# Kernel optimization log

Measured on AMD Instinct MI355X. Metric: run time of the kernel, lower is better.

The kernel has to match this reference:

```python
import jax, jax.numpy as jnp
import numpy as np

ROPE_BASE = 100.0  # CroCo/InfiniteVGGT-style 2D RoPE base

def _rope_1d(sub, pos, base=ROPE_BASE):
    # sub: (B,H,N,half), pos: (B,N) float
    half = sub.shape[-1]
    quarter = half // 2
    inv_freq = 1.0 / (base ** (jnp.arange(quarter, dtype=jnp.float32) / quarter))
    ang = pos[:, None, :, None] * inv_freq  # (B,1,N,quarter)
    cos, sin = jnp.cos(ang), jnp.sin(ang)
    x1, x2 = sub[..., :quarter], sub[..., quarter:]
    return jnp.concatenate([x1 * cos - x2 * sin, x1 * sin + x2 * cos], axis=-1)

def rope_2d(t, positions):
    # t: (B,H,N,Dh); positions: (B,N,2) int (y,x)
    Dh = t.shape[-1]
    half = Dh // 2
    pos_f = positions.astype(t.dtype)
    y = _rope_1d(t[..., :half], pos_f[..., 0])
    x = _rope_1d(t[..., half:], pos_f[..., 1])
    return jnp.concatenate([y, x], axis=-1)

def setup_inputs() -> dict:
    key = jax.random.key(0)
    k1, k2, k3, k4 = jax.random.split(key, 4)
    B, N, C, H = 2, 2048, 1024, 16
    x = jax.random.normal(k1, (B, N, C), dtype=jnp.float32)
    positions = jax.random.randint(k2, (B, N, 2), 0, 64, dtype=jnp.int32)
    qkv_w = jax.random.normal(k3, (3 * C, C), dtype=jnp.float32) * (C ** -0.5)
    proj_w = jax.random.normal(k4, (C, C), dtype=jnp.float32) * (C ** -0.5)
    proj_b = jnp.zeros((C,), dtype=jnp.float32)
    return {"x": x, "positions": positions, "qkv_w": qkv_w, "proj_w": proj_w, "proj_b": proj_b}

def reference(x, positions, qkv_w, proj_w, proj_b):
    B, N, C = x.shape
    H = 16
    Dh = C // H
    scale = Dh ** -0.5
    qkv = (x @ qkv_w.T).reshape(B, N, 3, H, Dh).transpose(2, 0, 3, 1, 4)  # (3,B,H,N,Dh)
    q, k, v = qkv[0], qkv[1], qkv[2]
    q = rope_2d(q, positions)
    k = rope_2d(k, positions)
    attn = jnp.einsum('bhnd,bhmd->bhnm', q, k) * scale  # (B,H,N,N)
    attn = jax.nn.softmax(attn, axis=-1)
    out = jnp.einsum('bhnm,bhmd->bhnd', attn, v)  # (B,H,N,Dh)
    out = out.transpose(0, 2, 1, 3).reshape(B, N, C)
    return out @ proj_w.T + proj_b
```

## Files before the change

### kernel.cpp

```cpp
#include <hip/hip_runtime.h>
#include <cmath>

typedef unsigned short u16;
typedef unsigned int   u32;
typedef __attribute__((ext_vector_type(8))) __bf16 bf16x8;
typedef __attribute__((ext_vector_type(2))) __bf16 bf16x2;
typedef __attribute__((ext_vector_type(4))) float  f32x4;
typedef __attribute__((ext_vector_type(2))) unsigned int u32x2;

constexpr int BB = 2, SEQ = 2048, CH = 1024, NH = 16, DH = 64;

__device__ inline u16 f2bf(float f) {
    u32 u = __builtin_bit_cast(u32, f);
    u += 0x7FFF + ((u >> 16) & 1);
    return (u16)(u >> 16);
}
__device__ inline float bf2f(u16 b) { return __builtin_bit_cast(float, (u32)b << 16); }
__device__ inline u32 pkbf(float a, float b) {
#if __has_builtin(__builtin_amdgcn_cvt_pk_bf16_f32)
    bf16x2 r = __builtin_amdgcn_cvt_pk_bf16_f32(a, b);
    return __builtin_bit_cast(u32, r);
#else
    return (u32)f2bf(a) | ((u32)f2bf(b) << 16);
#endif
}
__device__ inline float fexp2(float x) {
#if __has_builtin(__builtin_amdgcn_exp2f)
    return __builtin_amdgcn_exp2f(x);
#else
    return exp2f(x);
#endif
}

__device__ inline void pl32swap(u32& a, u32& b) {
#if __has_builtin(__builtin_amdgcn_permlane32_swap)
    u32x2 r = __builtin_amdgcn_permlane32_swap(a, b, false, false);
    a = r.x; b = r.y;
#else
    const int ln = threadIdx.x & 63;
    u32 ax = (u32)__shfl_xor((int)a, 32), bx = (u32)__shfl_xor((int)b, 32);
    u32 na = (ln & 32) ? bx : a;
    u32 nb = (ln & 32) ? b : ax;
    a = na; b = nb;
#endif
}
__device__ inline void pl16swap(u32& a, u32& b) {
#if __has_builtin(__builtin_amdgcn_permlane16_swap)
    u32x2 r = __builtin_amdgcn_permlane16_swap(a, b, false, false);
    a = r.x; b = r.y;
#else
    const int ln = threadIdx.x & 63;
    u32 ax = (u32)__shfl_xor((int)a, 16), bx = (u32)__shfl_xor((int)b, 16);
    u32 na = (ln & 16) ? bx : a;
    u32 nb = (ln & 16) ? b : ax;
    a = na; b = nb;
#endif
}

__device__ inline void gld_lds16(const void* g, void* l) {
    __builtin_amdgcn_global_load_lds((const __attribute__((address_space(1))) void*)g,
                                     (__attribute__((address_space(3))) void*)l, 16, 0, 0);
}
__device__ inline f32x4 mfma16(bf16x8 a, bf16x8 b, f32x4 c) {
    return __builtin_amdgcn_mfma_f32_16x16x32_bf16(a, b, c, 0, 0, 0);
}
__device__ inline bf16x8 ld_frag(const u16* p) {
    return __builtin_bit_cast(bf16x8, *(const uint4*)p);
}

__global__ __launch_bounds__(256) void convert_kernel(const float* __restrict__ x,
                                                      const float* __restrict__ wq,
                                                      const float* __restrict__ wp,
                                                      u16* __restrict__ xb,
                                                      u16* __restrict__ wqb,
                                                      u16* __restrict__ wpb,
                                                      float2* __restrict__ tabq,
                                                      float2* __restrict__ tabk) {
    const int q = blockIdx.x * 256 + threadIdx.x;
    if (q >= 2097152) {
        const int idx = q - 2097152;
        if (idx < 1024) {
            const int p = idx >> 4, i = idx & 15;
            const float f = exp2f(-(float)i * 0.41524101186092f);
            float s, c;
            sincosf((float)p * f, &s, &c);
            tabk[idx] = make_float2(c, s);
            tabq[idx] = make_float2(c * 0.18033688011112042f,
                                    s * 0.18033688011112042f);
        }
        return;
    }
    const float* src; u16* dst; int idx;
    if (q < 1048576)            { src = x;  dst = xb;  idx = q; }
    else if (q < 1048576+786432){ src = wq; dst = wqb; idx = q - 1048576; }
    else                        { src = wp; dst = wpb; idx = q - 1048576 - 786432; }
    float4 v = *(const float4*)(src + (size_t)idx * 4);
    ushort4 o; o.x = f2bf(v.x); o.y = f2bf(v.y); o.z = f2bf(v.z); o.w = f2bf(v.w);
    *(ushort4*)(dst + (size_t)idx * 4) = o;
}

__global__ __launch_bounds__(256) void gemm_qkv_rope(const u16* __restrict__ A,
                                                     const u16* __restrict__ Bw,
                                                     const int* __restrict__ pos,
                                                     const float2* __restrict__ tabq,
                                                     const float2* __restrict__ tabk,
                                                     u16* __restrict__ Qb,
                                                     u16* __restrict__ Kb,
                                                     u16* __restrict__ Vt) {
    __shared__ u16 smem[18432];
    const int t = threadIdx.x, lane = t & 63, w = t >> 6;
    const int l15 = lane & 15, quad = lane >> 4;
    const int wm = w >> 1, wn = w & 1;
    const int m0 = blockIdx.y * 128, n0 = blockIdx.x * 128;
    const int K = CH;

    const int row0 = t >> 2, v0 = t & 3;
    const int gi0 = (v0 - (row0 >> 1)) & 3;
    const int row1 = row0 + 64;
    const int gi1 = (v0 - (row1 >> 1)) & 3;

    const u16* A0 = A  + (size_t)(m0 + row0) * K + gi0 * 8;
    const u16* A1 = A  + (size_t)(m0 + row1) * K + gi1 * 8;
    const u16* B0 = Bw + (size_t)(n0 + row0) * K + gi0 * 8;
    const u16* B1 = Bw + (size_t)(n0 + row1) * K + gi1 * 8;

    gld_lds16(A0, smem + t * 8);
    gld_lds16(A1, smem + 2048 + t * 8);
    gld_lds16(B0, smem + 8192 + t * 8);
    gld_lds16(B1, smem + 10240 + t * 8);

    f32x4 acc[4][4] = {};
    for (int kt = 0; kt < K / 32; ++kt) {
        __syncthreads();
        const int cur = (kt & 1) * 4096;
        if (kt + 1 < K / 32) {
            const int off = (kt + 1) * 32;
            const int nxt = ((kt + 1) & 1) * 4096;
            gld_lds16(A0 + off, smem + nxt + t * 8);
            gld_lds16(A1 + off, smem + nxt + 2048 + t * 8);
            gld_lds16(B0 + off, smem + 8192 + nxt + t * 8);
            gld_lds16(B1 + off, smem + 8192 + nxt + 2048 + t * 8);
        }
        const u16* as = smem + cur;
        const u16* bs = smem + 8192 + cur;
        bf16x8 af[4], bfv[4];
#pragma unroll
        for (int mi = 0; mi < 4; ++mi) {
            const int r = wm * 64 + mi * 16 + l15;
            af[mi] = ld_frag(as + (r * 4 + ((quad + (r >> 1)) & 3)) * 8);
        }
#pragma unroll
        for (int nj = 0; nj < 4; ++nj) {
            const int r = wn * 64 + nj * 16 + l15;
            bfv[nj] = ld_frag(bs + (r * 4 + ((quad + (r >> 1)) & 3)) * 8);
        }
#pragma unroll
        for (int mi = 0; mi < 4; ++mi)
#pragma unroll
            for (int nj = 0; nj < 4; ++nj)
                acc[mi][nj] = mfma16(af[mi], bfv[nj], acc[mi][nj]);
    }

    const int reg = n0 >> 10;
    const int h   = ((n0 & 1023) >> 6) + wn;
    __syncthreads();
    u16* T = smem + w * 4608;
    const int rsel = lane >> 3, csel = lane & 7;
    if (reg < 2) {
        const float2* tab = reg ? tabk : tabq;
        u16* dstb = reg ? Kb : Qb;
#pragma unroll
        for (int mi = 0; mi < 4; ++mi) {
#pragma unroll
            for (int r = 0; r < 4; ++r) {
                const int m = m0 + wm * 64 + mi * 16 + quad * 4 + r;
                const int2 pp = *(const int2*)(pos + m * 2);
                const float2 ty = tab[pp.x * 16 + l15];
                const float2 tx = tab[pp.y * 16 + l15];
                const float x1 = acc[mi][0][r], x2 = acc[mi][1][r];
                const float y1 = acc[mi][2][r], y2 = acc[mi][3][r];
                const int ml = (mi * 16 + quad * 4 + r) * 72;
                T[ml + l15]      = f2bf(x1 * ty.x - x2 * ty.y);
                T[ml + l15 + 16] = f2bf(x1 * ty.y + x2 * ty.x);
                T[ml + l15 + 32] = f2bf(y1 * tx.x - y2 * tx.y);
                T[ml + l15 + 48] = f2bf(y1 * tx.y + y2 * tx.x);
            }
        }
        const int mbase = m0 + wm * 64;
        const int bh = (mbase >> 11) * NH + h;
        const int nbase = mbase & 2047;
#pragma unroll
        for (int j = 0; j < 8; ++j) {
            const int row = rsel + j * 8;
            u16* gp = dstb + ((size_t)bh * SEQ + nbase + row) * 64 + csel * 8;
            *(uint4*)gp = *(const uint4*)&T[row * 72 + csel * 8];
        }
    } else {
#pragma unroll
        for (int mi = 0; mi < 4; ++mi)
#pragma unroll
            for (int nj = 0; nj < 4; ++nj)
#pragma unroll
                for (int r = 0; r < 4; ++r)
                    T[(nj * 16 + l15) * 72 + mi * 16 + quad * 4 + r] =
                        f2bf(acc[mi][nj][r]);
        const int bh = (m0 >> 11) * NH + h;
        const int nbase = (m0 & 2047) + wm * 64;
#pragma unroll
        for (int j = 0; j < 8; ++j) {
            const int d = rsel + j * 8;
            u16* gp = Vt + ((size_t)bh * 64 + d) * SEQ + nbase + csel * 8;
            *(uint4*)gp = *(const uint4*)&T[d * 72 + csel * 8];
        }
    }
}

__global__ __launch_bounds__(256, 3) void attn_mfma(const u16* __restrict__ Qb,
                                                    const u16* __restrict__ Kb,
                                                    const u16* __restrict__ Vt,
                                                    u16* __restrict__ Opart,
                                                    float* __restrict__ lpart) {
    __shared__ u16 Ks[3][4096];
    __shared__ u16 Vs[3][4096];
    const int t = threadIdx.x, lane = t & 63, w = t >> 6;
    const int l15 = lane & 15, quad = lane >> 4;

    const int id = blockIdx.x;
    const int c  = id & 7, r_ = id >> 3;
    const int j  = r_ >> 4, xq = r_ & 15;
    const int g  = c + 8 * j;
    const int bh = g & 31;
    const int z  = g >> 5;
    const int q0 = xq * 128;

    const int rowA = t >> 3, vA = t & 7;
    const int giA = (vA - rowA) & 7;
    const int rowB = rowA + 32;
    const int giB = (vA - rowB) & 7;

    const size_t kbase = (size_t)bh * SEQ * 64;
    const size_t vbase = (size_t)bh * 64 * SEQ;

    const uint4 ones_u = {0x3F803F80u, 0x3F803F80u, 0x3F803F80u, 0x3F803F80u};
    const bf16x8 onesf = __builtin_bit_cast(bf16x8, ones_u);

    bf16x8 aq[2][2];
#pragma unroll
    for (int mi = 0; mi < 2; ++mi)
#pragma unroll
        for (int ks = 0; ks < 2; ++ks)
            aq[mi][ks] = ld_frag(Qb + ((size_t)bh * SEQ + q0 + w * 32 + mi * 16 + l15) * 64
                                 + ks * 32 + quad * 8);

#define STAGE(kt_, buf_)                                                          \
    {                                                                             \
        const int k0_ = z * 1024 + (kt_) * 64;                                    \
        gld_lds16(Kb + kbase + (size_t)(k0_ + rowA) * 64 + giA * 8,               \
                  &Ks[buf_][t * 8]);                                              \
        gld_lds16(Kb + kbase + (size_t)(k0_ + rowB) * 64 + giB * 8,               \
                  &Ks[buf_][2048 + t * 8]);                                       \
        gld_lds16(Vt + vbase + (size_t)rowA * SEQ + k0_ + giA * 8,                \
                  &Vs[buf_][t * 8]);                                              \
        gld_lds16(Vt + vbase + (size_t)rowB * SEQ + k0_ + giB * 8,                \
                  &Vs[buf_][2048 + t * 8]);                                       \
    }

    STAGE(0, 0)

    f32x4 oacc[2][4] = {};
    f32x4 lacc[2] = {};

    int rb = 0;
    for (int kt = 0; kt < 16; ++kt) {
        const int sb = (rb + 1 == 3) ? 0 : rb + 1;
        if (kt + 1 < 16) {
            STAGE(kt + 1, sb)
            asm volatile("s_waitcnt vmcnt(4)" ::: "memory");
        } else {
            asm volatile("s_waitcnt vmcnt(0)" ::: "memory");
        }
        __builtin_amdgcn_sched_barrier(0);
        __builtin_amdgcn_s_barrier();
        __builtin_amdgcn_sched_barrier(0);
        const u16* ksm = Ks[rb];
        const u16* vsm = Vs[rb];

        f32x4 sacc[2][4] = {};
        __builtin_amdgcn_s_setprio(1);
#pragma unroll
        for (int ks = 0; ks < 2; ++ks)
#pragma unroll
            for (int nk = 0; nk < 4; ++nk) {
                const int rK = nk * 16 + l15;
                const bf16x8 kf = ld_frag(ksm + (rK * 8 + (((ks * 4 + quad) + rK) & 7)) * 8);
                sacc[0][nk] = mfma16(kf, aq[0][ks], sacc[0][nk]);
                sacc[1][nk] = mfma16(kf, aq[1][ks], sacc[1][nk]);
            }
        __builtin_amdgcn_s_setprio(0);

        bf16x8 pa[2][2];
#pragma unroll
        for (int mi = 0; mi < 2; ++mi) {
            u32 W[4][2];
#pragma unroll
            for (int nk = 0; nk < 4; ++nk) {
                const float p0 = fexp2(sacc[mi][nk][0]);
                const float p1 = fexp2(sacc[mi][nk][1]);
                const float p2 = fexp2(sacc[mi][nk][2]);
                const float p3 = fexp2(sacc[mi][nk][3]);
                W[nk][0] = pkbf(p0, p1);
                W[nk][1] = pkbf(p2, p3);
            }
            u32 t0[4], t1[4];
            {
                u32 a = W[0][0], cc = W[1][0];
                pl32swap(a, cc); pl16swap(a, cc);
                t0[0] = a; t0[2] = cc;
            }
            {
                u32 a = W[0][1], cc = W[1][1];
                pl32swap(a, cc); pl16swap(a, cc);
                t0[1] = a; t0[3] = cc;
            }
            {
                u32 a = W[2][0], cc = W[3][0];
                pl32swap(a, cc); pl16swap(a, cc);
                t1[0] = a; t1[2] = cc;
            }
            {
                u32 a = W[2][1], cc = W[3][1];
                pl32swap(a, cc); pl16swap(a, cc);
                t1[1] = a; t1[3] = cc;
            }
            uint4 u0; u0.x = t0[0]; u0.y = t0[1]; u0.z = t0[2]; u0.w = t0[3];
            uint4 u1; u1.x = t1[0]; u1.y = t1[1]; u1.z = t1[2]; u1.w = t1[3];
            pa[mi][0] = __builtin_bit_cast(bf16x8, u0);
            pa[mi][1] = __builtin_bit_cast(bf16x8, u1);
        }

        __builtin_amdgcn_s_setprio(1);
        lacc[0] = mfma16(pa[0][0], onesf, lacc[0]);
        lacc[0] = mfma16(pa[0][1], onesf, lacc[0]);
        lacc[1] = mfma16(pa[1][0], onesf, lacc[1]);
        lacc[1] = mfma16(pa[1][1], onesf, lacc[1]);
#pragma unroll
        for (int ks = 0; ks < 2; ++ks)
#pragma unroll
            for (int nj = 0; nj < 4; ++nj) {
                const int rV = nj * 16 + l15;
                const bf16x8 vf = ld_frag(vsm + (rV * 8 + (((ks * 4 + quad) + rV) & 7)) * 8);
                oacc[0][nj] = mfma16(pa[0][ks], vf, oacc[0][nj]);
                oacc[1][nj] = mfma16(pa[1][ks], vf, oacc[1][nj]);
            }
        __builtin_amdgcn_s_setprio(0);
        rb = sb;
    }
#undef STAGE

    u16* ob = Opart + (size_t)z * 4194304;
#pragma unroll
    for (int mi = 0; mi < 2; ++mi)
#pragma unroll
        for (int r = 0; r < 4; ++r) {
            const int qrow = q0 + w * 32 + mi * 16 + quad * 4 + r;
            if (l15 == 0)
                lpart[((size_t)z * 32 + bh) * SEQ + qrow] = lacc[mi][r];
            const size_t orow = ((size_t)bh * SEQ + qrow) * 64;
#pragma unroll
            for (int nj = 0; nj < 4; ++nj)
                ob[orow + nj * 16 + l15] = f2bf(oacc[mi][nj][r]);
        }
}

__global__ __launch_bounds__(256) void merge_kernel(const u16* __restrict__ Opart,
                                                    const float* __restrict__ lpart,
                                                    u16* __restrict__ Ob) {
    const int gid = blockIdx.x * 256 + threadIdx.x;
    const int d4 = gid & 15, q = (gid >> 4) & 2047, bh = gid >> 15;
    const size_t i1 = ((size_t)bh * SEQ + q) * 64 + d4 * 4;
    const size_t i2 = i1 + 4194304;
    const float inv = 1.0f / (lpart[(size_t)bh * SEQ + q] +
                              lpart[((size_t)32 + bh) * SEQ + q]);
    const ushort4 a = *(const ushort4*)(Opart + i1);
    const ushort4 b = *(const ushort4*)(Opart + i2);
    ushort4 o;
    o.x = f2bf((bf2f(a.x) + bf2f(b.x)) * inv);
    o.y = f2bf((bf2f(a.y) + bf2f(b.y)) * inv);
    o.z = f2bf((bf2f(a.z) + bf2f(b.z)) * inv);
    o.w = f2bf((bf2f(a.w) + bf2f(b.w)) * inv);
    const int b_ = bh >> 4, h = bh & 15;
    *(ushort4*)(Ob + ((size_t)(b_ * SEQ + q)) * CH + h * 64 + d4 * 4) = o;
}

__global__ __launch_bounds__(256) void gemm_proj(const u16* __restrict__ A,
                                                 const u16* __restrict__ Bw,
                                                 const float* __restrict__ bias,
                                                 float* __restrict__ C) {
    __shared__ u16 smem[12288];
    const int t = threadIdx.x, lane = t & 63, w = t >> 6;
    const int l15 = lane & 15, quad = lane >> 4;
    const int wm = w >> 1, wn = w & 1;
    const int m0 = blockIdx.y * 64, n0 = blockIdx.x * 128;
    const int K = CH, N = CH;

    const int row0 = t >> 2, v0 = t & 3;
    const int gi0 = (v0 - (row0 >> 1)) & 3;
    const int row1 = row0 + 64;
    const int gi1 = (v0 - (row1 >> 1)) & 3;

    const u16* A0 = A  + (size_t)(m0 + row0) * K + gi0 * 8;
    const u16* B0 = Bw + (size_t)(n0 + row0) * K + gi0 * 8;
    const u16* B1 = Bw + (size_t)(n0 + row1) * K + gi1 * 8;

    gld_lds16(A0, smem + t * 8);
    gld_lds16(B0, smem + 4096 + t * 8);
    gld_lds16(B1, smem + 4096 + 2048 + t * 8);

    f32x4 acc[2][4] = {};
    for (int kt = 0; kt < K / 32; ++kt) {
        __syncthreads();
        const int curA = (kt & 1) * 2048;
        const int curB = 4096 + (kt & 1) * 4096;
        if (kt + 1 < K / 32) {
            const int off = (kt + 1) * 32;
            const int nxtA = ((kt + 1) & 1) * 2048;
            const int nxtB = 4096 + ((kt + 1) & 1) * 4096;
            gld_lds16(A0 + off, smem + nxtA + t * 8);
            gld_lds16(B0 + off, smem + nxtB + t * 8);
            gld_lds16(B1 + off, smem + nxtB + 2048 + t * 8);
        }
        const u16* as = smem + curA;
        const u16* bs = smem + curB;
        bf16x8 af[2], bfv[4];
#pragma unroll
        for (int mi = 0; mi < 2; ++mi) {
            const int r = wm * 32 + mi * 16 + l15;
            af[mi] = ld_frag(as + (r * 4 + ((quad + (r >> 1)) & 3)) * 8);
        }
#pragma unroll
        for (int nj = 0; nj < 4; ++nj) {
            const int r = wn * 64 + nj * 16 + l15;
            bfv[nj] = ld_frag(bs + (r * 4 + ((quad + (r >> 1)) & 3)) * 8);
        }
#pragma unroll
        for (int mi = 0; mi < 2; ++mi)
#pragma unroll
            for (int nj = 0; nj < 4; ++nj)
                acc[mi][nj] = mfma16(af[mi], bfv[nj], acc[mi][nj]);
    }
#pragma unroll
    for (int mi = 0; mi < 2; ++mi)
#pragma unroll
        for (int nj = 0; nj < 4; ++nj) {
            const int n = n0 + wn * 64 + nj * 16 + l15;
            const float bv = bias[n];
#pragma unroll
            for (int r = 0; r < 4; ++r) {
                const int m = m0 + wm * 32 + mi * 16 + quad * 4 + r;
                C[(size_t)m * N + n] = acc[mi][nj][r] + bv;
            }
        }
}

extern "C" void kernel_launch(void* const* d_in, const int* in_sizes, int n_in,
                              void* d_out, int out_size, void* d_ws, size_t ws_size,
                              hipStream_t stream) {
    const float* x      = (const float*)d_in[0];
    const int*   pos    = (const int*)d_in[1];
    const float* qkv_w  = (const float*)d_in[2];
    const float* proj_w = (const float*)d_in[3];
    const float* proj_b = (const float*)d_in[4];
    float* out = (float*)d_out;

    u16* ws = (u16*)d_ws;
    u16* x_bf    = ws;
    u16* attn_bf = ws;
    u16* wq_bf   = ws + 4194304;
    float* lpart = (float*)(ws + 4194304);
    u16* wp_bf   = ws + 7340032;
    u16* Qb      = ws + 8388608;
    u16* Kb      = ws + 12582912;
    u16* Vt      = ws + 16777216;
    u16* Opart   = ws + 20971520;
    float2* tabq = (float2*)(ws + 20971520);
    float2* tabk = (float2*)(ws + 20971520 + 4096);

    const int M = BB * SEQ;

    convert_kernel<<<8196, 256, 0, stream>>>(x, qkv_w, proj_w, x_bf, wq_bf, wp_bf,
                                             tabq, tabk);
    gemm_qkv_rope<<<dim3(3 * CH / 128, M / 128), 256, 0, stream>>>(
        x_bf, wq_bf, pos, tabq, tabk, Qb, Kb, Vt);
    attn_mfma<<<1024, 256, 0, stream>>>(Qb, Kb, Vt, Opart, lpart);
    merge_kernel<<<4096, 256, 0, stream>>>(Opart, lpart, attn_bf);
    gemm_proj<<<dim3(CH / 128, M / 64), 256, 0, stream>>>(
        attn_bf, wp_bf, proj_b, out);
}
```

Baseline: 199.4 us.

## Drop split-K attention and merge kernel, normalize output inside attention

The attention kernel no longer splits the 2048 keys into two halves with separate partial outputs. Each block now walks all 32 key tiles, divides by its own row sum and writes the bf16 result straight into the (B,N,C) layout that the projection GEMM reads. This removes the merge kernel launch and the write-then-read of partial outputs and row sums through global memory. In exchange the attention grid halves to 512 blocks, which may leave compute units underfilled and makes each block run twice as long.

```diff
diff --git a/kernel.cpp b/kernel.cpp
--- a/kernel.cpp
+++ b/kernel.cpp
@@ -218,8 +218,7 @@
 __global__ __launch_bounds__(256, 3) void attn_mfma(const u16* __restrict__ Qb,
                                                     const u16* __restrict__ Kb,
                                                     const u16* __restrict__ Vt,
-                                                    u16* __restrict__ Opart,
-                                                    float* __restrict__ lpart) {
+                                                    u16* __restrict__ Ob) {
     __shared__ u16 Ks[3][4096];
     __shared__ u16 Vs[3][4096];
     const int t = threadIdx.x, lane = t & 63, w = t >> 6;
@@ -228,9 +227,7 @@
     const int id = blockIdx.x;
     const int c  = id & 7, r_ = id >> 3;
     const int j  = r_ >> 4, xq = r_ & 15;
-    const int g  = c + 8 * j;
-    const int bh = g & 31;
-    const int z  = g >> 5;
+    const int bh = c + 8 * j;
     const int q0 = xq * 128;
 
     const int rowA = t >> 3, vA = t & 7;
@@ -254,7 +251,7 @@
 
 #define STAGE(kt_, buf_)                                                          \
     {                                                                             \
-        const int k0_ = z * 1024 + (kt_) * 64;                                    \
+        const int k0_ = (kt_) * 64;                                               \
         gld_lds16(Kb + kbase + (size_t)(k0_ + rowA) * 64 + giA * 8,               \
                   &Ks[buf_][t * 8]);                                              \
         gld_lds16(Kb + kbase + (size_t)(k0_ + rowB) * 64 + giB * 8,               \
@@ -271,9 +268,9 @@
     f32x4 lacc[2] = {};
 
     int rb = 0;
-    for (int kt = 0; kt < 16; ++kt) {
+    for (int kt = 0; kt < 32; ++kt) {
         const int sb = (rb + 1 == 3) ? 0 : rb + 1;
-        if (kt + 1 < 16) {
+        if (kt + 1 < 32) {
             STAGE(kt + 1, sb)
             asm volatile("s_waitcnt vmcnt(4)" ::: "memory");
         } else {
@@ -357,39 +354,18 @@
     }
 #undef STAGE
 
-    u16* ob = Opart + (size_t)z * 4194304;
+    const int b_ = bh >> 4, h = bh & 15;
 #pragma unroll
     for (int mi = 0; mi < 2; ++mi)
 #pragma unroll
         for (int r = 0; r < 4; ++r) {
             const int qrow = q0 + w * 32 + mi * 16 + quad * 4 + r;
-            if (l15 == 0)
-                lpart[((size_t)z * 32 + bh) * SEQ + qrow] = lacc[mi][r];
-            const size_t orow = ((size_t)bh * SEQ + qrow) * 64;
+            const float inv = 1.0f / lacc[mi][r];
+            u16* gp = Ob + ((size_t)(b_ * SEQ + qrow)) * CH + h * 64;
 #pragma unroll
             for (int nj = 0; nj < 4; ++nj)
-                ob[orow + nj * 16 + l15] = f2bf(oacc[mi][nj][r]);
-        }
-}
-
-__global__ __launch_bounds__(256) void merge_kernel(const u16* __restrict__ Opart,
-                                                    const float* __restrict__ lpart,
-                                                    u16* __restrict__ Ob) {
-    const int gid = blockIdx.x * 256 + threadIdx.x;
-    const int d4 = gid & 15, q = (gid >> 4) & 2047, bh = gid >> 15;
-    const size_t i1 = ((size_t)bh * SEQ + q) * 64 + d4 * 4;
-    const size_t i2 = i1 + 4194304;
-    const float inv = 1.0f / (lpart[(size_t)bh * SEQ + q] +
-                              lpart[((size_t)32 + bh) * SEQ + q]);
-    const ushort4 a = *(const ushort4*)(Opart + i1);
-    const ushort4 b = *(const ushort4*)(Opart + i2);
-    ushort4 o;
-    o.x = f2bf((bf2f(a.x) + bf2f(b.x)) * inv);
-    o.y = f2bf((bf2f(a.y) + bf2f(b.y)) * inv);
-    o.z = f2bf((bf2f(a.z) + bf2f(b.z)) * inv);
-    o.w = f2bf((bf2f(a.w) + bf2f(b.w)) * inv);
-    const int b_ = bh >> 4, h = bh & 15;
-    *(ushort4*)(Ob + ((size_t)(b_ * SEQ + q)) * CH + h * 64 + d4 * 4) = o;
+                gp[nj * 16 + l15] = f2bf(oacc[mi][nj][r] * inv);
+        }
 }
 
 __global__ __launch_bounds__(256) void gemm_proj(const u16* __restrict__ A,
@@ -476,12 +452,10 @@
     u16* x_bf    = ws;
     u16* attn_bf = ws;
     u16* wq_bf   = ws + 4194304;
-    float* lpart = (float*)(ws + 4194304);
     u16* wp_bf   = ws + 7340032;
     u16* Qb      = ws + 8388608;
     u16* Kb      = ws + 12582912;
     u16* Vt      = ws + 16777216;
-    u16* Opart   = ws + 20971520;
     float2* tabq = (float2*)(ws + 20971520);
     float2* tabk = (float2*)(ws + 20971520 + 4096);
 
@@ -491,8 +465,7 @@
                                              tabq, tabk);
     gemm_qkv_rope<<<dim3(3 * CH / 128, M / 128), 256, 0, stream>>>(
         x_bf, wq_bf, pos, tabq, tabk, Qb, Kb, Vt);
-    attn_mfma<<<1024, 256, 0, stream>>>(Qb, Kb, Vt, Opart, lpart);
-    merge_kernel<<<4096, 256, 0, stream>>>(Opart, lpart, attn_bf);
+    attn_mfma<<<512, 256, 0, stream>>>(Qb, Kb, Vt, attn_bf);
     gemm_proj<<<dim3(CH / 128, M / 64), 256, 0, stream>>>(
         attn_bf, wp_bf, proj_b, out);
 }
```

Measured after the change: 194.3 us. 1.03x faster.
